# Performance work log

Measured on AMD Instinct MI355X. Metric: run time of the kernel, lower is better.

The kernel has to match this reference:

```python
import jax, jax.numpy as jnp
import numpy as np

N_EMBD = 1024
N_HEAD = 16
HEAD_SIZE = 64
LN_EPS = 1e-3  # keras LayerNormalization default


def setup_inputs() -> dict:
    key = jax.random.key(0)
    ks = jax.random.split(key, 7)
    B, S, D, H, E = 4, 2048, N_EMBD, N_HEAD, HEAD_SIZE
    x = jax.random.normal(ks[0], (B, S, D), dtype=jnp.float32)
    scale = 1.0 / np.sqrt(D)
    Wq = jax.random.normal(ks[1], (H, D, E), dtype=jnp.float32) * scale
    Wk = jax.random.normal(ks[2], (H, D, E), dtype=jnp.float32) * scale
    Wv = jax.random.normal(ks[3], (H, D, E), dtype=jnp.float32) * scale
    Wo = jax.random.normal(ks[4], (H * E, D), dtype=jnp.float32) * scale
    gamma = jnp.ones((D,), dtype=jnp.float32)
    beta = jnp.zeros((D,), dtype=jnp.float32)
    return {"x": x, "Wq": Wq, "Wk": Wk, "Wv": Wv, "Wo": Wo,
            "gamma": gamma, "beta": beta}


def reference(x, Wq, Wk, Wv, Wo, gamma, beta):
    B, S, D = x.shape
    H, _, E = Wq.shape
    q = jnp.einsum('bsd,hde->bhse', x, Wq)
    k = jnp.einsum('bsd,hde->bhse', x, Wk)
    v = jnp.einsum('bsd,hde->bhse', x, Wv)
    scores = jnp.einsum('bhse,bhte->bhst', q, k)  # [B,H,S,S]
    causal = jnp.tril(jnp.ones((S, S), dtype=bool))
    # original: mask with -inf, then divide by sqrt(head_size) -> same result
    scores = jnp.where(causal, scores / jnp.sqrt(jnp.float32(E)),
                       jnp.float32(-jnp.inf))
    attn = jax.nn.softmax(scores, axis=-1)
    out = jnp.einsum('bhst,bhte->bhse', attn, v)
    heads = out.transpose(0, 2, 1, 3).reshape(B, S, H * E)  # concat heads
    y = x + heads @ Wo
    # keras LayerNormalization (axis=-1, eps=1e-3)
    mu = jnp.mean(y, axis=-1, keepdims=True)
    var = jnp.mean(jnp.square(y - mu), axis=-1, keepdims=True)
    y = (y - mu) * jax.lax.rsqrt(var + LN_EPS) * gamma + beta
    return y
```

## Files before the change

### kernel.cpp

```cpp
#include <hip/hip_runtime.h>
#include <stdint.h>

typedef __bf16 bf16;
typedef float  f32x4  __attribute__((ext_vector_type(4)));
typedef float  float4v __attribute__((ext_vector_type(4)));
typedef bf16   bf16x8 __attribute__((ext_vector_type(8)));
typedef bf16   bf16x4 __attribute__((ext_vector_type(4)));

#define B_ 4
#define S_ 2048
#define D_ 1024
#define H_ 16
#define E_ 64
#define M_ 8192
#define QSCALE 0.18033688f


__device__ __forceinline__ void async_ld16(const bf16* g, bf16* l) {
  __builtin_amdgcn_global_load_lds(
      (const __attribute__((address_space(1))) void*)g,
      (__attribute__((address_space(3))) void*)l, 16, 0, 0);
}


__global__ __launch_bounds__(256) void pack_x(const float* __restrict__ x,
                                              bf16* __restrict__ xb, int n4) {
  int i = blockIdx.x * 256 + threadIdx.x;
  if (i < n4) {
    float4v v = ((const float4v*)x)[i];
    bf16x4 o = { (bf16)v.x, (bf16)v.y, (bf16)v.z, (bf16)v.w };
    ((bf16x4*)xb)[i] = o;
  }
}

__global__ __launch_bounds__(256) void pack_wqkv(const float* __restrict__ Wq,
                                                 const float* __restrict__ Wk,
                                                 const float* __restrict__ Wv,
                                                 bf16* __restrict__ Bt) {
  __shared__ float t[64][65];
  const int mat = blockIdx.x;
  const int qkv = mat >> 4, h = mat & 15;
  const float* W = (qkv == 0) ? Wq : ((qkv == 1) ? Wk : Wv);
  const float* src = W + h * (D_ * E_);
  const int d0 = blockIdx.y * 64;
  const int tr = threadIdx.x >> 2;
  const int tc = (threadIdx.x & 3) * 16;
  for (int i = 0; i < 16; ++i) t[tr][tc + i] = src[(d0 + tr) * E_ + tc + i];
  __syncthreads();
  const int n = qkv * 1024 + h * 64 + tr;
  bf16* dst = Bt + n * D_ + d0 + tc;
  for (int i = 0; i < 16; ++i) dst[i] = (bf16)t[tc + i][tr];
}

__global__ __launch_bounds__(256) void pack_wo(const float* __restrict__ Wo,
                                               bf16* __restrict__ Wot) {
  __shared__ float t[64][65];
  const int k0 = blockIdx.x * 64, n0 = blockIdx.y * 64;
  const int tr = threadIdx.x >> 2;
  const int tc = (threadIdx.x & 3) * 16;
  for (int i = 0; i < 16; ++i) t[tr][tc + i] = Wo[(k0 + tr) * D_ + n0 + tc + i];
  __syncthreads();
  bf16* dst = Wot + (n0 + tr) * D_ + k0 + tc;
  for (int i = 0; i < 16; ++i) dst[i] = (bf16)t[tc + i][tr];
}


template <int EPI>
__global__ __launch_bounds__(256, 2) void gemm128(
    const bf16* __restrict__ A, const bf16* __restrict__ Bt, int K,
    bf16* __restrict__ qo, bf16* __restrict__ ko, bf16* __restrict__ vt,
    const float* __restrict__ xres, float* __restrict__ outp) {
  __shared__ bf16 As[128 * 64];
  __shared__ bf16 Bs[128 * 64];
  const int tid = threadIdx.x;
  const int wave = tid >> 6, lane = tid & 63;
  const int lm = lane & 15, quad = lane >> 4;
  const int wr = wave >> 1, wc = wave & 1;
  const int m0 = blockIdx.y * 128, n0 = blockIdx.x * 128;
  f32x4 acc[4][4] = {};

  for (int kt = 0; kt < K; kt += 64) {
    for (int it = 0; it < 4; ++it) {
      int cl = it * 256 + tid;
      int r = cl >> 3, pc = cl & 7;
      int cc = pc ^ (r & 7);
      async_ld16(A + (m0 + r) * K + kt + cc * 8, As + cl * 8);
      async_ld16(Bt + (n0 + r) * K + kt + cc * 8, Bs + cl * 8);
    }
    __syncthreads();
    for (int kk = 0; kk < 64; kk += 32) {
      bf16x8 af[4], bfr[4];
      const int ccb = (kk >> 3) + quad;
      for (int i = 0; i < 4; ++i) {
        int row = wr * 64 + i * 16 + lm;
        af[i] = *(const bf16x8*)(As + row * 64 + (ccb ^ (row & 7)) * 8);
      }
      for (int j = 0; j < 4; ++j) {
        int row = wc * 64 + j * 16 + lm;
        bfr[j] = *(const bf16x8*)(Bs + row * 64 + (ccb ^ (row & 7)) * 8);
      }
      for (int i = 0; i < 4; ++i)
        for (int j = 0; j < 4; ++j)
          acc[i][j] = __builtin_amdgcn_mfma_f32_16x16x32_bf16(af[i], bfr[j], acc[i][j], 0, 0, 0);
    }
    __syncthreads();
  }

  if (EPI == 0) {
    const int qkv = n0 >> 10;
    const int hh = ((n0 + wc * 64) >> 6) & 15;
    for (int i = 0; i < 4; ++i) {
      const int gm0 = m0 + wr * 64 + i * 16 + quad * 4;
      const int b = gm0 >> 11, s0 = gm0 & 2047;
      for (int j = 0; j < 4; ++j) {
        const int e = j * 16 + lm;
        if (qkv == 2) {
          bf16x4 pv = { (bf16)acc[i][j][0], (bf16)acc[i][j][1],
                        (bf16)acc[i][j][2], (bf16)acc[i][j][3] };
          *(bf16x4*)(vt + (((b << 4) + hh) * 64 + e) * (size_t)S_ + s0) = pv;
        } else if (qkv == 0) {
          for (int r = 0; r < 4; ++r)
            qo[(((b << 4) + hh) * S_ + (s0 + r)) * (size_t)E_ + e] =
                (bf16)(acc[i][j][r] * QSCALE);
        } else {
          for (int r = 0; r < 4; ++r)
            ko[(((b << 4) + hh) * S_ + (s0 + r)) * (size_t)E_ + e] = (bf16)acc[i][j][r];
        }
      }
    }
  } else {
    for (int i = 0; i < 4; ++i)
      for (int r = 0; r < 4; ++r) {
        const int gm = m0 + wr * 64 + i * 16 + quad * 4 + r;
        for (int j = 0; j < 4; ++j) {
          const int gn = n0 + wc * 64 + j * 16 + lm;
          outp[gm * (size_t)D_ + gn] = acc[i][j][r] + xres[gm * (size_t)D_ + gn];
        }
      }
  }
}


__global__ __launch_bounds__(512, 4) void attn(
    const bf16* __restrict__ Q, const bf16* __restrict__ Kb,
    const bf16* __restrict__ Vt, bf16* __restrict__ Hd) {
  __shared__ __align__(16) bf16 Ks[2][64 * 64];
  __shared__ __align__(16) bf16 Vs[2][64 * 64];
  __shared__ __align__(16) bf16 Pb[8][16 * 64];
  const int tid = threadIdx.x;
  const int w = tid >> 6, lane = tid & 63;
  const int lm = lane & 15, quad = lane >> 4;
  const int l7 = lm & 7;
  const int bi = blockIdx.x;
  const int bh = bi & 63;
  const int At = bi >> 6;
  const bf16* Qp = Q + (size_t)bh * S_ * E_;
  const bf16* Kp = Kb + (size_t)bh * S_ * E_;
  const bf16* Vp = Vt + (size_t)bh * E_ * S_;

  int qb[2], sq[2];
  bf16x8 qf[2][2];
  qb[0] = At * 128 + w * 16;
  qb[1] = (15 - At) * 128 + w * 16;
#pragma unroll
  for (int t = 0; t < 2; ++t) {
    sq[t] = qb[t] + lm;
    qf[t][0] = *(const bf16x8*)(Qp + sq[t] * E_ + quad * 8);
    qf[t][1] = *(const bf16x8*)(Qp + sq[t] * E_ + 32 + quad * 8);
  }
  float ls[2] = { 0.0f, 0.0f };
  f32x4 oacc[2][4] = {};

  const int jmax = 31 - 2 * At;
  for (int j = 0; j <= jmax; ++j) {
    const int p = j & 1;
    const int sk0 = j * 64;
    {
      int cl = tid;
      int r = cl >> 3, pc = cl & 7;
      int cc = pc ^ (r & 7);
      async_ld16(Kp + (sk0 + r) * E_ + cc * 8, &Ks[p][cl * 8]);
      async_ld16(Vp + (size_t)r * S_ + sk0 + cc * 8, &Vs[p][cl * 8]);
    }
    __syncthreads();

#pragma unroll
    for (int t = 0; t < 2; ++t) {
      const int d = (qb[t] - sk0) >> 4;
      if (d < 0) continue;
      f32x4 st[4] = {};
#pragma unroll
      for (int i = 0; i < 4; ++i) {
        const int row = i * 16 + lm;
        bf16x8 k0 = *(const bf16x8*)(&Ks[p][row * 64 + (quad ^ l7) * 8]);
        st[i] = __builtin_amdgcn_mfma_f32_16x16x32_bf16(k0, qf[t][0], st[i], 0, 0, 0);
        bf16x8 k1 = *(const bf16x8*)(&Ks[p][row * 64 + ((4 + quad) ^ l7) * 8]);
        st[i] = __builtin_amdgcn_mfma_f32_16x16x32_bf16(k1, qf[t][1], st[i], 0, 0, 0);
      }
      if (d < 4) {
#pragma unroll
        for (int i = 0; i < 4; ++i) {
          const int base = (i - d) * 16 + quad * 4;
#pragma unroll
          for (int r = 0; r < 4; ++r)
            st[i][r] = (base + r > lm) ? -30000.0f : st[i][r];
        }
      }
      char* pbase = (char*)&Pb[w][0];
#pragma unroll
      for (int i = 0; i < 4; ++i) {
        const float p0 = __builtin_amdgcn_exp2f(st[i][0]);
        const float p1 = __builtin_amdgcn_exp2f(st[i][1]);
        const float p2 = __builtin_amdgcn_exp2f(st[i][2]);
        const float p3 = __builtin_amdgcn_exp2f(st[i][3]);
        ls[t] += (p0 + p1) + (p2 + p3);
        bf16x4 pv = { (bf16)p0, (bf16)p1, (bf16)p2, (bf16)p3 };
        const int c = (i * 2 + (quad >> 1)) ^ l7;
        *(bf16x4*)(pbase + lm * 128 + c * 16 + (quad & 1) * 8) = pv;
      }
#pragma unroll
      for (int ks = 0; ks < 2; ++ks) {
        bf16x8 pf = *(const bf16x8*)(pbase + lm * 128 + ((ks * 4 + quad) ^ l7) * 16);
#pragma unroll
        for (int te = 0; te < 4; ++te) {
          const int vrow = te * 16 + lm;
          bf16x8 vf = *(const bf16x8*)(&Vs[p][vrow * 64 + ((ks * 4 + quad) ^ l7) * 8]);
          oacc[t][te] = __builtin_amdgcn_mfma_f32_16x16x32_bf16(vf, pf, oacc[t][te], 0, 0, 0);
        }
      }
    }
  }
  const int b = bh >> 4, h = bh & 15;
#pragma unroll
  for (int t = 0; t < 2; ++t) {
    float rs = ls[t];
    rs += __shfl_xor(rs, 16);
    rs += __shfl_xor(rs, 32);
    const float inv = 1.0f / rs;
#pragma unroll
    for (int te = 0; te < 4; ++te) {
      bf16x4 ov = { (bf16)(oacc[t][te][0] * inv), (bf16)(oacc[t][te][1] * inv),
                    (bf16)(oacc[t][te][2] * inv), (bf16)(oacc[t][te][3] * inv) };
      *(bf16x4*)(&Hd[((size_t)b * S_ + sq[t]) * D_ + h * 64 + te * 16 + quad * 4]) = ov;
    }
  }
}


__global__ __launch_bounds__(256) void lnorm(float* __restrict__ y,
                                             const float* __restrict__ gamma,
                                             const float* __restrict__ beta) {
  const int row = blockIdx.x, tid = threadIdx.x;
  float4v v = ((const float4v*)y)[row * 256 + tid];
  float s = v.x + v.y + v.z + v.w;
  float ss = v.x * v.x + v.y * v.y + v.z * v.z + v.w * v.w;
#pragma unroll
  for (int o = 1; o < 64; o <<= 1) { s += __shfl_xor(s, o); ss += __shfl_xor(ss, o); }
  __shared__ float sb[8];
  const int wv = tid >> 6, lane = tid & 63;
  if (lane == 0) { sb[wv] = s; sb[4 + wv] = ss; }
  __syncthreads();
  s = sb[0] + sb[1] + sb[2] + sb[3];
  ss = sb[4] + sb[5] + sb[6] + sb[7];
  const float mu = s * (1.0f / 1024.0f);
  const float var = ss * (1.0f / 1024.0f) - mu * mu;
  const float rstd = rsqrtf(var + 1e-3f);
  float4v g = ((const float4v*)gamma)[tid];
  float4v bb = ((const float4v*)beta)[tid];
  float4v o;
  o.x = (v.x - mu) * rstd * g.x + bb.x;
  o.y = (v.y - mu) * rstd * g.y + bb.y;
  o.z = (v.z - mu) * rstd * g.z + bb.z;
  o.w = (v.w - mu) * rstd * g.w + bb.w;
  ((float4v*)y)[row * 256 + tid] = o;
}


extern "C" void kernel_launch(void* const* d_in, const int* in_sizes, int n_in,
                              void* d_out, int out_size, void* d_ws, size_t ws_size,
                              hipStream_t stream) {
  const float* x     = (const float*)d_in[0];
  const float* Wq    = (const float*)d_in[1];
  const float* Wk    = (const float*)d_in[2];
  const float* Wv    = (const float*)d_in[3];
  const float* Wo    = (const float*)d_in[4];
  const float* gamma = (const float*)d_in[5];
  const float* beta  = (const float*)d_in[6];
  float* out = (float*)d_out;

  char* ws = (char*)d_ws;
  bf16* xb    = (bf16*)(ws);
  bf16* wqkvt = (bf16*)(ws + 16777216);
  bf16* wot   = (bf16*)(ws + 23068672);
  bf16* Qb    = (bf16*)(ws + 25165824);
  bf16* Kb    = (bf16*)(ws + 41943040);
  bf16* Vtb   = (bf16*)(ws + 58720256);
  bf16* heads = xb;

  pack_x<<<M_ * D_ / 4 / 256, 256, 0, stream>>>(x, xb, M_ * D_ / 4);
  pack_wqkv<<<dim3(48, 16), 256, 0, stream>>>(Wq, Wk, Wv, wqkvt);
  pack_wo<<<dim3(16, 16), 256, 0, stream>>>(Wo, wot);
  gemm128<0><<<dim3(24, 64), 256, 0, stream>>>(xb, wqkvt, D_, Qb, Kb, Vtb, nullptr, nullptr);
  attn<<<64 * 8, 512, 0, stream>>>(Qb, Kb, Vtb, heads);
  gemm128<1><<<dim3(8, 64), 256, 0, stream>>>(heads, wot, D_, nullptr, nullptr, nullptr, x, out);
  lnorm<<<M_, 256, 0, stream>>>(out, gamma, beta);
}
```

Baseline: 260.1 us.

## Widen attention key tile to 128, read V from global, merge pack kernels

The attention kernel now processes 128 keys per iteration instead of 64, which halves the number of loop iterations and block barriers. Only K is staged in LDS through async loads. V fragments are loaded straight from global memory inside the PV loop, so all eight waves re-read the same V tile through the caches. The three packing kernels are merged into one launch that branches on block index, removing two kernel launches. The trade-offs are more LDS per block for the larger K and P buffers, more registers for the wider score tile, and V loads that are exposed in the inner loop without LDS staging.

```diff
diff --git a/kernel.cpp b/kernel.cpp
--- a/kernel.cpp
+++ b/kernel.cpp
@@ -23,45 +23,42 @@
 }
 
 
-__global__ __launch_bounds__(256) void pack_x(const float* __restrict__ x,
-                                              bf16* __restrict__ xb, int n4) {
-  int i = blockIdx.x * 256 + threadIdx.x;
-  if (i < n4) {
+__global__ __launch_bounds__(256) void packs(
+    const float* __restrict__ x, const float* __restrict__ Wq,
+    const float* __restrict__ Wk, const float* __restrict__ Wv,
+    const float* __restrict__ Wo, bf16* __restrict__ xb,
+    bf16* __restrict__ Bt, bf16* __restrict__ Wot) {
+  __shared__ float t[64][65];
+  const int bid = blockIdx.x;
+  if (bid < 8192) {
+    int i = bid * 256 + threadIdx.x;
     float4v v = ((const float4v*)x)[i];
     bf16x4 o = { (bf16)v.x, (bf16)v.y, (bf16)v.z, (bf16)v.w };
     ((bf16x4*)xb)[i] = o;
-  }
-}
-
-__global__ __launch_bounds__(256) void pack_wqkv(const float* __restrict__ Wq,
-                                                 const float* __restrict__ Wk,
-                                                 const float* __restrict__ Wv,
-                                                 bf16* __restrict__ Bt) {
-  __shared__ float t[64][65];
-  const int mat = blockIdx.x;
-  const int qkv = mat >> 4, h = mat & 15;
-  const float* W = (qkv == 0) ? Wq : ((qkv == 1) ? Wk : Wv);
-  const float* src = W + h * (D_ * E_);
-  const int d0 = blockIdx.y * 64;
+    return;
+  }
   const int tr = threadIdx.x >> 2;
   const int tc = (threadIdx.x & 3) * 16;
-  for (int i = 0; i < 16; ++i) t[tr][tc + i] = src[(d0 + tr) * E_ + tc + i];
-  __syncthreads();
-  const int n = qkv * 1024 + h * 64 + tr;
-  bf16* dst = Bt + n * D_ + d0 + tc;
-  for (int i = 0; i < 16; ++i) dst[i] = (bf16)t[tc + i][tr];
-}
-
-__global__ __launch_bounds__(256) void pack_wo(const float* __restrict__ Wo,
-                                               bf16* __restrict__ Wot) {
-  __shared__ float t[64][65];
-  const int k0 = blockIdx.x * 64, n0 = blockIdx.y * 64;
-  const int tr = threadIdx.x >> 2;
-  const int tc = (threadIdx.x & 3) * 16;
-  for (int i = 0; i < 16; ++i) t[tr][tc + i] = Wo[(k0 + tr) * D_ + n0 + tc + i];
-  __syncthreads();
-  bf16* dst = Wot + (n0 + tr) * D_ + k0 + tc;
-  for (int i = 0; i < 16; ++i) dst[i] = (bf16)t[tc + i][tr];
+  if (bid < 8960) {
+    const int fb = bid - 8192;
+    const int mat = fb % 48;
+    const int d0 = (fb / 48) * 64;
+    const int qkv = mat >> 4, h = mat & 15;
+    const float* W = (qkv == 0) ? Wq : ((qkv == 1) ? Wk : Wv);
+    const float* src = W + h * (D_ * E_);
+    for (int i = 0; i < 16; ++i) t[tr][tc + i] = src[(d0 + tr) * E_ + tc + i];
+    __syncthreads();
+    const int n = qkv * 1024 + h * 64 + tr;
+    bf16* dst = Bt + n * D_ + d0 + tc;
+    for (int i = 0; i < 16; ++i) dst[i] = (bf16)t[tc + i][tr];
+  } else {
+    const int fb = bid - 8960;
+    const int k0 = (fb & 15) * 64, n0 = (fb >> 4) * 64;
+    for (int i = 0; i < 16; ++i) t[tr][tc + i] = Wo[(k0 + tr) * D_ + n0 + tc + i];
+    __syncthreads();
+    bf16* dst = Wot + (n0 + tr) * D_ + k0 + tc;
+    for (int i = 0; i < 16; ++i) dst[i] = (bf16)t[tc + i][tr];
+  }
 }
 
 
@@ -144,9 +141,8 @@
 __global__ __launch_bounds__(512, 4) void attn(
     const bf16* __restrict__ Q, const bf16* __restrict__ Kb,
     const bf16* __restrict__ Vt, bf16* __restrict__ Hd) {
-  __shared__ __align__(16) bf16 Ks[2][64 * 64];
-  __shared__ __align__(16) bf16 Vs[2][64 * 64];
-  __shared__ __align__(16) bf16 Pb[8][16 * 64];
+  __shared__ __align__(16) bf16 Ks[2][128 * 64];
+  __shared__ __align__(16) bf16 Pb[8][16 * 128];
   const int tid = threadIdx.x;
   const int w = tid >> 6, lane = tid & 63;
   const int lm = lane & 15, quad = lane >> 4;
@@ -171,16 +167,16 @@
   float ls[2] = { 0.0f, 0.0f };
   f32x4 oacc[2][4] = {};
 
-  const int jmax = 31 - 2 * At;
+  const int jmax = 15 - At;
   for (int j = 0; j <= jmax; ++j) {
     const int p = j & 1;
-    const int sk0 = j * 64;
-    {
-      int cl = tid;
+    const int sk0 = j * 128;
+#pragma unroll
+    for (int it = 0; it < 2; ++it) {
+      int cl = it * 512 + tid;
       int r = cl >> 3, pc = cl & 7;
       int cc = pc ^ (r & 7);
       async_ld16(Kp + (sk0 + r) * E_ + cc * 8, &Ks[p][cl * 8]);
-      async_ld16(Vp + (size_t)r * S_ + sk0 + cc * 8, &Vs[p][cl * 8]);
     }
     __syncthreads();
 
@@ -188,18 +184,18 @@
     for (int t = 0; t < 2; ++t) {
       const int d = (qb[t] - sk0) >> 4;
       if (d < 0) continue;
-      f32x4 st[4] = {};
-#pragma unroll
-      for (int i = 0; i < 4; ++i) {
+      f32x4 st[8] = {};
+#pragma unroll
+      for (int i = 0; i < 8; ++i) {
         const int row = i * 16 + lm;
         bf16x8 k0 = *(const bf16x8*)(&Ks[p][row * 64 + (quad ^ l7) * 8]);
         st[i] = __builtin_amdgcn_mfma_f32_16x16x32_bf16(k0, qf[t][0], st[i], 0, 0, 0);
         bf16x8 k1 = *(const bf16x8*)(&Ks[p][row * 64 + ((4 + quad) ^ l7) * 8]);
         st[i] = __builtin_amdgcn_mfma_f32_16x16x32_bf16(k1, qf[t][1], st[i], 0, 0, 0);
       }
-      if (d < 4) {
-#pragma unroll
-        for (int i = 0; i < 4; ++i) {
+      if (d < 8) {
+#pragma unroll
+        for (int i = 0; i < 8; ++i) {
           const int base = (i - d) * 16 + quad * 4;
 #pragma unroll
           for (int r = 0; r < 4; ++r)
@@ -208,7 +204,7 @@
       }
       char* pbase = (char*)&Pb[w][0];
 #pragma unroll
-      for (int i = 0; i < 4; ++i) {
+      for (int i = 0; i < 8; ++i) {
         const float p0 = __builtin_amdgcn_exp2f(st[i][0]);
         const float p1 = __builtin_amdgcn_exp2f(st[i][1]);
         const float p2 = __builtin_amdgcn_exp2f(st[i][2]);
@@ -216,15 +212,15 @@
         ls[t] += (p0 + p1) + (p2 + p3);
         bf16x4 pv = { (bf16)p0, (bf16)p1, (bf16)p2, (bf16)p3 };
         const int c = (i * 2 + (quad >> 1)) ^ l7;
-        *(bf16x4*)(pbase + lm * 128 + c * 16 + (quad & 1) * 8) = pv;
-      }
-#pragma unroll
-      for (int ks = 0; ks < 2; ++ks) {
-        bf16x8 pf = *(const bf16x8*)(pbase + lm * 128 + ((ks * 4 + quad) ^ l7) * 16);
+        *(bf16x4*)(pbase + lm * 256 + c * 16 + (quad & 1) * 8) = pv;
+      }
+#pragma unroll
+      for (int ks = 0; ks < 4; ++ks) {
+        bf16x8 pf = *(const bf16x8*)(pbase + lm * 256 + ((ks * 4 + quad) ^ l7) * 16);
 #pragma unroll
         for (int te = 0; te < 4; ++te) {
           const int vrow = te * 16 + lm;
-          bf16x8 vf = *(const bf16x8*)(&Vs[p][vrow * 64 + ((ks * 4 + quad) ^ l7) * 8]);
+          bf16x8 vf = *(const bf16x8*)(Vp + (size_t)vrow * S_ + sk0 + ks * 32 + quad * 8);
           oacc[t][te] = __builtin_amdgcn_mfma_f32_16x16x32_bf16(vf, pf, oacc[t][te], 0, 0, 0);
         }
       }
@@ -297,9 +293,7 @@
   bf16* Vtb   = (bf16*)(ws + 58720256);
   bf16* heads = xb;
 
-  pack_x<<<M_ * D_ / 4 / 256, 256, 0, stream>>>(x, xb, M_ * D_ / 4);
-  pack_wqkv<<<dim3(48, 16), 256, 0, stream>>>(Wq, Wk, Wv, wqkvt);
-  pack_wo<<<dim3(16, 16), 256, 0, stream>>>(Wo, wot);
+  packs<<<9216, 256, 0, stream>>>(x, Wq, Wk, Wv, Wo, xb, wqkvt, wot);
   gemm128<0><<<dim3(24, 64), 256, 0, stream>>>(xb, wqkvt, D_, Qb, Kb, Vtb, nullptr, nullptr);
   attn<<<64 * 8, 512, 0, stream>>>(Qb, Kb, Vtb, heads);
   gemm128<1><<<dim3(8, 64), 256, 0, stream>>>(heads, wot, D_, nullptr, nullptr, nullptr, x, out);
```

New measurement: 357.2 us. 37.4% more time.
